# Kernel optimization log

Hardware: AMD Instinct MI355X
Metric: run time of the kernel (lower is better)

## Reference

```python
import jax, jax.numpy as jnp
import numpy as np


def setup_inputs() -> dict:
    key = jax.random.key(0)
    ks = jax.random.split(key, 16)
    B, S, H = 512, 128, 256
    f32 = jnp.float32
    inputs = jax.random.normal(ks[0], (B, S, 2), f32)
    # xavier-normal-ish init (gain/sqrt(fan_in+fan_out) approximated by small scale)
    def xn(k, shape):
        fan = shape[0] + shape[1]
        return jax.random.normal(k, shape, f32) * np.sqrt(2.0 / fan)
    return {
        "inputs": inputs,
        "W0": xn(ks[1], (H, 2)),   "b0": jnp.zeros((H,), f32),
        "W1": xn(ks[2], (H, H)),   "b1": jnp.zeros((H,), f32),
        "W2": xn(ks[3], (H, H)),   "b2": jnp.zeros((H,), f32),
        "W3": xn(ks[4], (H, H)),   "b3": jnp.zeros((H,), f32),
        "W4": xn(ks[5], (1, H)),   "b4": jnp.zeros((1,), f32),
        "log_growth_rate": jax.random.normal(ks[6], (), f32),
        "log_carrying_capacity": jax.random.normal(ks[7], (), f32),
        "log_initial_loss": jax.random.normal(ks[8], (), f32),
        "in_mean": jnp.array([0.5, 50.0], f32),
        "in_std": jnp.array([0.2, 30.0], f32),
        "tgt_mean": jnp.array([0.8], f32),
        "tgt_std": jnp.array([0.1], f32),
    }


def reference(inputs, W0, b0, W1, b1, W2, b2, W3, b3, W4, b4,
              log_growth_rate, log_carrying_capacity, log_initial_loss,
              in_mean, in_std, tgt_mean, tgt_std):
    B, S = inputs.shape[0], inputs.shape[1]
    # PDE parameters (Verhulst logistic growth)
    r = jnp.exp(-log_growth_rate)
    K = 0.2 + (1.0 - 0.2) * jax.nn.sigmoid(log_carrying_capacity)  # carrying capacity in [0.2, 1]
    C = 0.0 + (0.1 - 0.0) * jax.nn.sigmoid(log_initial_loss)       # initial loss in [0, 0.1]

    # split state feature s and time t, standardize per-column
    s = inputs[..., 0:1].reshape(-1, 1)  # [N,1]
    t = inputs[..., 1:2].reshape(-1, 1)  # [N,1]
    s_norm = (s - in_mean[0:1]) / (in_std[0:1] + 1e-8)
    t_norm = (t - in_mean[1:2]) / (in_std[1:2] + 1e-8)

    Ws = (W0, W1, W2, W3, W4)
    bs = (b0, b1, b2, b3, b4)

    def mlp(x):  # [N,2] -> [N,1], tanh MLP
        h = x
        for W, b in zip(Ws[:-1], bs[:-1]):
            h = jnp.tanh(h @ W.T + b)
        return h @ Ws[-1].T + bs[-1]

    def u_of(tn):  # U(s_norm, tn), inverse-standardized targets
        return mlp(jnp.concatenate([s_norm, tn], axis=-1)) * tgt_std + tgt_mean

    ones = jnp.ones_like(t_norm)

    def uf_of(tn):
        # U and U_t = dU/dt_norm (forward-mode; each point depends on its own scalar t)
        U, U_dot = jax.jvp(u_of, (tn,), (ones,))
        U_t = U_dot.sum(-1, keepdims=True)
        G = r * (U - C) * (1.0 - (U - C) / (K - C))  # Verhulst
        return U, U_t - G  # (U, F)

    # second derivative w.r.t. t_norm: F_t = U_tt - G_t
    (U, F), (_, F_t) = jax.jvp(uf_of, (t_norm,), (ones,))

    shp = (B, S, 1)
    return U.reshape(shp), F.reshape(shp), F_t.reshape(shp)
```

## Files before the change

kernel.cpp:

```cpp
#include <hip/hip_runtime.h>
#include <hip/hip_bf16.h>
#include <math.h>

typedef short s8v __attribute__((ext_vector_type(8)));
typedef float f4v __attribute__((ext_vector_type(4)));

#define HH 256
#define TP 32
#define NTHREADS 256
#define KSTR 520
#define TSTR 4160
#define NTILES 6
#define PLANE (NTILES * TSTR)

__device__ __forceinline__ unsigned short bf_rne(float x){
    union{float f;unsigned u;}v; v.f=x;
    unsigned r = v.u + 0x7FFFu + ((v.u >> 16) & 1u);
    return (unsigned short)(r >> 16);
}
__device__ __forceinline__ unsigned pack_rne2(float a, float b){
    union { __hip_bfloat162 h; unsigned u; } v;
    v.h = __float22bfloat162_rn(float2{a, b});
    return v.u;
}

__global__ __launch_bounds__(256)
void prep_weights(const float* __restrict__ W1, const float* __restrict__ W2,
                  const float* __restrict__ W3, const float* __restrict__ W0,
                  const float* __restrict__ b0, const float* __restrict__ W4,
                  unsigned short* __restrict__ wsB, float* __restrict__ wsF)
{
    int t = blockIdx.x * 256 + threadIdx.x;
    if (t < 24576) {
        int layer = t >> 13;
        int rem = t & 8191;
        int l  = rem & 63;
        int ks = (rem >> 6) & 7;
        int nt = rem >> 9;
        const float* W = (layer == 0) ? W1 : (layer == 1) ? W2 : W3;
        int n_out = nt * 16 + (l & 15);
        int quad  = l >> 4;
        const float* row = W + n_out * HH;
        s8v hi;
        #pragma unroll
        for (int j = 0; j < 8; ++j) {
            int n_in = quad * 64 + (j & 3) * 16 + ((j >> 2) << 3) + ks;
            hi[j] = (short)bf_rne(row[n_in]);
        }
        int dst = ((nt * 8 + ks) * 64 + l) * 8;
        *(s8v*)(wsB + layer * 65536 + dst) = hi;
    } else if (t < 24832) {
        int n = t - 24576;
        int pos = ((n & 7) * 4 + (n >> 6)) * 8 + ((n >> 4) & 3) + 4 * ((n >> 3) & 1);
        wsF[pos]       = W0[2 * n];
        wsF[256 + pos] = W0[2 * n + 1];
        wsF[512 + pos] = b0[n];
        wsF[768 + pos] = W4[n];
    }
}

__global__ __launch_bounds__(NTHREADS, 3)
void capnn_mfma(const float* __restrict__ inp,
                const float* __restrict__ b1, const float* __restrict__ b2,
                const float* __restrict__ b3, const float* __restrict__ b4,
                const float* __restrict__ W4raw,
                const float* __restrict__ lgr, const float* __restrict__ lcc,
                const float* __restrict__ lil,
                const float* __restrict__ imean, const float* __restrict__ istd,
                const float* __restrict__ tmean, const float* __restrict__ tstd,
                const unsigned short* __restrict__ wsW,
                const float* __restrict__ wsF,
                float* __restrict__ out, int N)
{
    __shared__ __align__(16) unsigned short Ahi[PLANE];
    __shared__ float sn_sh[TP], tn_sh[TP];
    __shared__ float head_part[TP * 3 * 4];

    const int tid  = threadIdx.x;
    const int lane = tid & 63;
    const int w    = tid >> 6;
    const int m16  = lane & 15;
    const int q    = lane >> 4;
    const int pbase = blockIdx.x * TP;

    const float* __restrict__ w00p = wsF;
    const float* __restrict__ w01p = wsF + 256;
    const float* __restrict__ b0p  = wsF + 512;

    float w4v[4];
    #pragma unroll
    for (int i = 0; i < 4; ++i) w4v[i] = W4raw[w * 64 + i * 16 + m16];

    if (tid < TP) {
        int pg = pbase + tid;
        float s = 0.f, t = 0.f;
        if (pg < N) { s = inp[2 * pg]; t = inp[2 * pg + 1]; }
        sn_sh[tid] = (s - imean[0]) / (istd[0] + 1e-8f);
        tn_sh[tid] = (t - imean[1]) / (istd[1] + 1e-8f);
    }
    __syncthreads();

    {
        const int l  = tid & 63;
        const int wv = tid >> 6;
        const int p16 = l & 15, quad = l >> 4;
        #pragma unroll
        for (int g2 = 0; g2 < 2; ++g2) {
            const int ks = wv + 4 * g2;
            const int pos = (ks * 4 + quad) * 8;
            float4 wA0 = *(const float4*)(w00p + pos);
            float4 wA1 = *(const float4*)(w00p + pos + 4);
            float4 wB0 = *(const float4*)(w01p + pos);
            float4 wB1 = *(const float4*)(w01p + pos + 4);
            float4 bb0 = *(const float4*)(b0p + pos);
            float4 bb1 = *(const float4*)(b0p + pos + 4);
            float w00v[8] = {wA0.x,wA0.y,wA0.z,wA0.w,wA1.x,wA1.y,wA1.z,wA1.w};
            float w01v[8] = {wB0.x,wB0.y,wB0.z,wB0.w,wB1.x,wB1.y,wB1.z,wB1.w};
            float b0v[8]  = {bb0.x,bb0.y,bb0.z,bb0.w,bb1.x,bb1.y,bb1.z,bb1.w};
            const int base = ks * KSTR + l * 8;
            #pragma unroll
            for (int h = 0; h < 2; ++h) {
                const float sn = sn_sh[h * 16 + p16], tn = tn_sh[h * 16 + p16];
                float av[8], d1v[8], d2v[8];
                #pragma unroll
                for (int j = 0; j < 8; ++j) {
                    float z = fmaf(w00v[j], sn, fmaf(w01v[j], tn, b0v[j]));
                    float e = __expf(2.f * z);
                    float a = 1.f - 2.f * __builtin_amdgcn_rcpf(e + 1.f);
                    float g = 1.f - a * a;
                    float d1 = g * w01v[j];
                    float d2 = -2.f * a * d1 * w01v[j];
                    av[j] = a; d1v[j] = d1; d2v[j] = d2;
                }
                #pragma unroll
                for (int s = 0; s < 3; ++s) {
                    const float* V = (s == 0) ? av : (s == 1) ? d1v : d2v;
                    int4 hi4;
                    hi4.x = (int)pack_rne2(V[0], V[1]);
                    hi4.y = (int)pack_rne2(V[2], V[3]);
                    hi4.z = (int)pack_rne2(V[4], V[5]);
                    hi4.w = (int)pack_rne2(V[6], V[7]);
                    *(int4*)&Ahi[(s * 2 + h) * TSTR + base] = hi4;
                }
            }
        }
    }
    __syncthreads();

    for (int L = 0; L < 3; ++L) {
        const unsigned short* __restrict__ Wlh = wsW + L * 65536;
        const float* __restrict__ bL = (L == 0) ? b1 : (L == 1) ? b2 : b3;

        f4v acc[NTILES][4];
        #pragma unroll
        for (int i = 0; i < 4; ++i) {
            float bias = bL[w * 64 + i * 16 + m16];
            acc[0][i] = (f4v){bias, bias, bias, bias};
            acc[1][i] = (f4v){bias, bias, bias, bias};
            #pragma unroll
            for (int t = 2; t < NTILES; ++t)
                acc[t][i] = (f4v){0.f, 0.f, 0.f, 0.f};
        }

        #pragma unroll
        for (int ks = 0; ks < 8; ++ks) {
            s8v ah[NTILES];
            const int aoff = ks * KSTR + lane * 8;
            #pragma unroll
            for (int t = 0; t < NTILES; ++t)
                ah[t] = *(const s8v*)&Ahi[t * TSTR + aoff];
            #pragma unroll
            for (int i = 0; i < 4; ++i) {
                const int off = (((w * 4 + i) * 8 + ks) * 64 + lane) * 8;
                s8v bh = *(const s8v*)(Wlh + off);
                #pragma unroll
                for (int t = 0; t < NTILES; ++t)
                    acc[t][i] = __builtin_amdgcn_mfma_f32_16x16x32_bf16(ah[t], bh, acc[t][i], 0, 0, 0);
            }
        }

        if (L < 2) {
            __syncthreads();
            const int ksw  = m16 & 7;
            const int hsel = m16 >> 3;
            const int wbase = ksw * KSTR + (16 * w + q * 4) * 8 + 4 * hsel;
            #pragma unroll
            for (int h = 0; h < 2; ++h) {
                #pragma unroll
                for (int r = 0; r < 4; ++r) {
                    float Av[3][4];
                    #pragma unroll
                    for (int i = 0; i < 4; ++i) {
                        float z  = acc[h][i][r];
                        float z1 = acc[2 + h][i][r];
                        float z2 = acc[4 + h][i][r];
                        float e = __expf(2.f * z);
                        float a = 1.f - 2.f * __builtin_amdgcn_rcpf(e + 1.f);
                        float g = 1.f - a * a;
                        float d1 = g * z1;
                        float d2 = fmaf(g, z2, -2.f * a * d1 * z1);
                        Av[0][i] = a; Av[1][i] = d1; Av[2][i] = d2;
                    }
                    #pragma unroll
                    for (int s = 0; s < 3; ++s) {
                        int2 hi2;
                        hi2.x = (int)pack_rne2(Av[s][0], Av[s][1]);
                        hi2.y = (int)pack_rne2(Av[s][2], Av[s][3]);
                        *(int2*)&Ahi[(s * 2 + h) * TSTR + wbase + r * 8] = hi2;
                    }
                }
            }
            __syncthreads();
        } else {
            float hp[3][2][4];
            #pragma unroll
            for (int s = 0; s < 3; ++s)
                #pragma unroll
                for (int h = 0; h < 2; ++h)
                    #pragma unroll
                    for (int r = 0; r < 4; ++r) hp[s][h][r] = 0.f;
            #pragma unroll
            for (int h = 0; h < 2; ++h) {
                #pragma unroll
                for (int r = 0; r < 4; ++r) {
                    #pragma unroll
                    for (int i = 0; i < 4; ++i) {
                        float z  = acc[h][i][r];
                        float z1 = acc[2 + h][i][r];
                        float z2 = acc[4 + h][i][r];
                        float e = __expf(2.f * z);
                        float a = 1.f - 2.f * __builtin_amdgcn_rcpf(e + 1.f);
                        float g = 1.f - a * a;
                        float d1 = g * z1;
                        float d2 = fmaf(g, z2, -2.f * a * d1 * z1);
                        hp[0][h][r] = fmaf(w4v[i], a,  hp[0][h][r]);
                        hp[1][h][r] = fmaf(w4v[i], d1, hp[1][h][r]);
                        hp[2][h][r] = fmaf(w4v[i], d2, hp[2][h][r]);
                    }
                }
            }
            #pragma unroll
            for (int m = 1; m < 16; m <<= 1) {
                #pragma unroll
                for (int s = 0; s < 3; ++s)
                    #pragma unroll
                    for (int h = 0; h < 2; ++h)
                        #pragma unroll
                        for (int r = 0; r < 4; ++r)
                            hp[s][h][r] += __shfl_xor(hp[s][h][r], m);
            }
            if (m16 == 0) {
                #pragma unroll
                for (int s = 0; s < 3; ++s)
                    #pragma unroll
                    for (int h = 0; h < 2; ++h)
                        #pragma unroll
                        for (int r = 0; r < 4; ++r)
                            head_part[(s * TP + h * 16 + q * 4 + r) * 4 + w] = hp[s][h][r];
            }
            __syncthreads();
        }
    }

    if (tid < TP) {
        float sv = 0.f, s1v = 0.f, s2v = 0.f;
        #pragma unroll
        for (int ww = 0; ww < 4; ++ww) {
            sv  += head_part[(0 * TP + tid) * 4 + ww];
            s1v += head_part[(1 * TP + tid) * 4 + ww];
            s2v += head_part[(2 * TP + tid) * 4 + ww];
        }
        int pg = pbase + tid;
        if (pg < N) {
            float r_  = expf(-lgr[0]);
            float Kc  = 0.2f + 0.8f / (1.f + expf(-lcc[0]));
            float Cc  = 0.1f / (1.f + expf(-lil[0]));
            float kci = 1.f / (Kc - Cc);
            float ts = tstd[0], tm = tmean[0];
            float U   = (sv + b4[0]) * ts + tm;
            float Ut  = s1v * ts;
            float Utt = s2v * ts;
            float Um  = U - Cc;
            float G   = r_ * Um * (1.f - Um * kci);
            float Gt  = r_ * Ut * (1.f - 2.f * Um * kci);
            out[pg]         = U;
            out[N + pg]     = Ut - G;
            out[2 * N + pg] = Utt - Gt;
        }
    }
}

extern "C" void kernel_launch(void* const* d_in, const int* in_sizes, int n_in,
                              void* d_out, int out_size, void* d_ws, size_t ws_size,
                              hipStream_t stream) {
    const float* inp   = (const float*)d_in[0];
    const float* W0    = (const float*)d_in[1];
    const float* b0    = (const float*)d_in[2];
    const float* W1    = (const float*)d_in[3];
    const float* b1    = (const float*)d_in[4];
    const float* W2    = (const float*)d_in[5];
    const float* b2    = (const float*)d_in[6];
    const float* W3    = (const float*)d_in[7];
    const float* b3    = (const float*)d_in[8];
    const float* W4    = (const float*)d_in[9];
    const float* b4    = (const float*)d_in[10];
    const float* lgr   = (const float*)d_in[11];
    const float* lcc   = (const float*)d_in[12];
    const float* lil   = (const float*)d_in[13];
    const float* imean = (const float*)d_in[14];
    const float* istd  = (const float*)d_in[15];
    const float* tmean = (const float*)d_in[16];
    const float* tstd  = (const float*)d_in[17];

    unsigned short* wsB = (unsigned short*)d_ws;
    float* wsF = (float*)((char*)d_ws + 393216);

    const int N = in_sizes[0] / 2;
    const int gridMain = (N + TP - 1) / TP;

    hipLaunchKernelGGL(prep_weights, dim3(97), dim3(256), 0, stream,
                       W1, W2, W3, W0, b0, W4, wsB, wsF);
    hipLaunchKernelGGL(capnn_mfma, dim3(gridMain), dim3(NTHREADS), 0, stream,
                       inp, b1, b2, b3, b4, W4,
                       lgr, lcc, lil, imean, istd, tmean, tstd,
                       wsB, wsF, (float*)d_out, N);
}
```

Baseline: 176.4 us.

## Ping-pong two wave sets staggered by one phase to overlap MFMA and tanh

The block now has 512 threads in two sets of four waves, each set working on its own 32-point tile with its own LDS plane. The sets run the layer schedule one phase apart, so one set's MFMA GEMM runs while the other does tanh/derivative elementwise work, and GEMM phases raise wave priority with s_setprio. This is meant to fill MFMA idle time during the transcendental-heavy epilogues, at the cost of double LDS use, lower declared occupancy (2 blocks) and a barrier every phase.

After: 184.8 us. 4.7% more time.

```diff
diff --git a/kernel.cpp b/kernel.cpp
--- a/kernel.cpp
+++ b/kernel.cpp
@@ -6,8 +6,9 @@
 typedef float f4v __attribute__((ext_vector_type(4)));
 
 #define HH 256
-#define TP 32
-#define NTHREADS 256
+#define TPS 32
+#define TP 64
+#define NTHREADS 512
 #define KSTR 520
 #define TSTR 4160
 #define NTILES 6
@@ -59,7 +60,7 @@
     }
 }
 
-__global__ __launch_bounds__(NTHREADS, 3)
+__global__ __launch_bounds__(NTHREADS, 2)
 void capnn_mfma(const float* __restrict__ inp,
                 const float* __restrict__ b1, const float* __restrict__ b2,
                 const float* __restrict__ b3, const float* __restrict__ b4,
@@ -72,27 +73,26 @@
                 const float* __restrict__ wsF,
                 float* __restrict__ out, int N)
 {
-    __shared__ __align__(16) unsigned short Ahi[PLANE];
+    __shared__ __align__(16) unsigned short Ahi[2 * PLANE];
     __shared__ float sn_sh[TP], tn_sh[TP];
-    __shared__ float head_part[TP * 3 * 4];
+    __shared__ float head_part[2][TPS * 3 * 4];
 
     const int tid  = threadIdx.x;
     const int lane = tid & 63;
     const int w    = tid >> 6;
+    const int set  = w >> 2;
+    const int wl   = w & 3;
     const int m16  = lane & 15;
     const int q    = lane >> 4;
-    const int pbase = blockIdx.x * TP;
+
+    unsigned short* const plane = Ahi + set * PLANE;
 
     const float* __restrict__ w00p = wsF;
     const float* __restrict__ w01p = wsF + 256;
     const float* __restrict__ b0p  = wsF + 512;
 
-    float w4v[4];
-    #pragma unroll
-    for (int i = 0; i < 4; ++i) w4v[i] = W4raw[w * 64 + i * 16 + m16];
-
     if (tid < TP) {
-        int pg = pbase + tid;
+        int pg = blockIdx.x * TP + tid;
         float s = 0.f, t = 0.f;
         if (pg < N) { s = inp[2 * pg]; t = inp[2 * pg + 1]; }
         sn_sh[tid] = (s - imean[0]) / (istd[0] + 1e-8f);
@@ -100,90 +100,93 @@
     }
     __syncthreads();
 
-    {
-        const int l  = tid & 63;
-        const int wv = tid >> 6;
-        const int p16 = l & 15, quad = l >> 4;
-        #pragma unroll
-        for (int g2 = 0; g2 < 2; ++g2) {
-            const int ks = wv + 4 * g2;
-            const int pos = (ks * 4 + quad) * 8;
-            float4 wA0 = *(const float4*)(w00p + pos);
-            float4 wA1 = *(const float4*)(w00p + pos + 4);
-            float4 wB0 = *(const float4*)(w01p + pos);
-            float4 wB1 = *(const float4*)(w01p + pos + 4);
-            float4 bb0 = *(const float4*)(b0p + pos);
-            float4 bb1 = *(const float4*)(b0p + pos + 4);
-            float w00v[8] = {wA0.x,wA0.y,wA0.z,wA0.w,wA1.x,wA1.y,wA1.z,wA1.w};
-            float w01v[8] = {wB0.x,wB0.y,wB0.z,wB0.w,wB1.x,wB1.y,wB1.z,wB1.w};
-            float b0v[8]  = {bb0.x,bb0.y,bb0.z,bb0.w,bb1.x,bb1.y,bb1.z,bb1.w};
-            const int base = ks * KSTR + l * 8;
-            #pragma unroll
-            for (int h = 0; h < 2; ++h) {
-                const float sn = sn_sh[h * 16 + p16], tn = tn_sh[h * 16 + p16];
-                float av[8], d1v[8], d2v[8];
-                #pragma unroll
-                for (int j = 0; j < 8; ++j) {
-                    float z = fmaf(w00v[j], sn, fmaf(w01v[j], tn, b0v[j]));
-                    float e = __expf(2.f * z);
-                    float a = 1.f - 2.f * __builtin_amdgcn_rcpf(e + 1.f);
-                    float g = 1.f - a * a;
-                    float d1 = g * w01v[j];
-                    float d2 = -2.f * a * d1 * w01v[j];
-                    av[j] = a; d1v[j] = d1; d2v[j] = d2;
+    f4v acc[NTILES][4];
+
+    #pragma unroll 1
+    for (int iv = 0; iv < 8; ++iv) {
+        const int ph = iv - set;
+
+        if (ph == 0) {
+            const int l = lane;
+            const int p16 = l & 15, quad = l >> 4;
+            #pragma unroll
+            for (int g2 = 0; g2 < 2; ++g2) {
+                const int ks = wl + 4 * g2;
+                const int pos = (ks * 4 + quad) * 8;
+                float4 wA0 = *(const float4*)(w00p + pos);
+                float4 wA1 = *(const float4*)(w00p + pos + 4);
+                float4 wB0 = *(const float4*)(w01p + pos);
+                float4 wB1 = *(const float4*)(w01p + pos + 4);
+                float4 bb0 = *(const float4*)(b0p + pos);
+                float4 bb1 = *(const float4*)(b0p + pos + 4);
+                float w00v[8] = {wA0.x,wA0.y,wA0.z,wA0.w,wA1.x,wA1.y,wA1.z,wA1.w};
+                float w01v[8] = {wB0.x,wB0.y,wB0.z,wB0.w,wB1.x,wB1.y,wB1.z,wB1.w};
+                float b0v[8]  = {bb0.x,bb0.y,bb0.z,bb0.w,bb1.x,bb1.y,bb1.z,bb1.w};
+                const int base = ks * KSTR + l * 8;
+                #pragma unroll
+                for (int h = 0; h < 2; ++h) {
+                    const float sn = sn_sh[set * TPS + h * 16 + p16];
+                    const float tn = tn_sh[set * TPS + h * 16 + p16];
+                    float av[8], d1v[8], d2v[8];
+                    #pragma unroll
+                    for (int j = 0; j < 8; ++j) {
+                        float z = fmaf(w00v[j], sn, fmaf(w01v[j], tn, b0v[j]));
+                        float e = __expf(2.f * z);
+                        float a = 1.f - 2.f * __builtin_amdgcn_rcpf(e + 1.f);
+                        float g = 1.f - a * a;
+                        float d1 = g * w01v[j];
+                        float d2 = -2.f * a * d1 * w01v[j];
+                        av[j] = a; d1v[j] = d1; d2v[j] = d2;
+                    }
+                    #pragma unroll
+                    for (int s = 0; s < 3; ++s) {
+                        const float* V = (s == 0) ? av : (s == 1) ? d1v : d2v;
+                        int4 hi4;
+                        hi4.x = (int)pack_rne2(V[0], V[1]);
+                        hi4.y = (int)pack_rne2(V[2], V[3]);
+                        hi4.z = (int)pack_rne2(V[4], V[5]);
+                        hi4.w = (int)pack_rne2(V[6], V[7]);
+                        *(int4*)&plane[(s * 2 + h) * TSTR + base] = hi4;
+                    }
                 }
-                #pragma unroll
-                for (int s = 0; s < 3; ++s) {
-                    const float* V = (s == 0) ? av : (s == 1) ? d1v : d2v;
-                    int4 hi4;
-                    hi4.x = (int)pack_rne2(V[0], V[1]);
-                    hi4.y = (int)pack_rne2(V[2], V[3]);
-                    hi4.z = (int)pack_rne2(V[4], V[5]);
-                    hi4.w = (int)pack_rne2(V[6], V[7]);
-                    *(int4*)&Ahi[(s * 2 + h) * TSTR + base] = hi4;
+            }
+        } else if (ph == 1 || ph == 3 || ph == 5) {
+            const int L = (ph - 1) >> 1;
+            const unsigned short* __restrict__ Wlh = wsW + L * 65536;
+            const float* __restrict__ bL = (L == 0) ? b1 : (L == 1) ? b2 : b3;
+
+            #pragma unroll
+            for (int i = 0; i < 4; ++i) {
+                float bias = bL[wl * 64 + i * 16 + m16];
+                acc[0][i] = (f4v){bias, bias, bias, bias};
+                acc[1][i] = (f4v){bias, bias, bias, bias};
+                #pragma unroll
+                for (int t = 2; t < NTILES; ++t)
+                    acc[t][i] = (f4v){0.f, 0.f, 0.f, 0.f};
+            }
+
+            __builtin_amdgcn_s_setprio(1);
+            #pragma unroll
+            for (int ks = 0; ks < 8; ++ks) {
+                s8v ah[NTILES];
+                const int aoff = ks * KSTR + lane * 8;
+                #pragma unroll
+                for (int t = 0; t < NTILES; ++t)
+                    ah[t] = *(const s8v*)&plane[t * TSTR + aoff];
+                #pragma unroll
+                for (int i = 0; i < 4; ++i) {
+                    const int off = (((wl * 4 + i) * 8 + ks) * 64 + lane) * 8;
+                    s8v bh = *(const s8v*)(Wlh + off);
+                    #pragma unroll
+                    for (int t = 0; t < NTILES; ++t)
+                        acc[t][i] = __builtin_amdgcn_mfma_f32_16x16x32_bf16(ah[t], bh, acc[t][i], 0, 0, 0);
                 }
             }
-        }
-    }
-    __syncthreads();
-
-    for (int L = 0; L < 3; ++L) {
-        const unsigned short* __restrict__ Wlh = wsW + L * 65536;
-        const float* __restrict__ bL = (L == 0) ? b1 : (L == 1) ? b2 : b3;
-
-        f4v acc[NTILES][4];
-        #pragma unroll
-        for (int i = 0; i < 4; ++i) {
-            float bias = bL[w * 64 + i * 16 + m16];
-            acc[0][i] = (f4v){bias, bias, bias, bias};
-            acc[1][i] = (f4v){bias, bias, bias, bias};
-            #pragma unroll
-            for (int t = 2; t < NTILES; ++t)
-                acc[t][i] = (f4v){0.f, 0.f, 0.f, 0.f};
-        }
-
-        #pragma unroll
-        for (int ks = 0; ks < 8; ++ks) {
-            s8v ah[NTILES];
-            const int aoff = ks * KSTR + lane * 8;
-            #pragma unroll
-            for (int t = 0; t < NTILES; ++t)
-                ah[t] = *(const s8v*)&Ahi[t * TSTR + aoff];
-            #pragma unroll
-            for (int i = 0; i < 4; ++i) {
-                const int off = (((w * 4 + i) * 8 + ks) * 64 + lane) * 8;
-                s8v bh = *(const s8v*)(Wlh + off);
-                #pragma unroll
-                for (int t = 0; t < NTILES; ++t)
-                    acc[t][i] = __builtin_amdgcn_mfma_f32_16x16x32_bf16(ah[t], bh, acc[t][i], 0, 0, 0);
-            }
-        }
-
-        if (L < 2) {
-            __syncthreads();
+            __builtin_amdgcn_s_setprio(0);
+        } else if (ph == 2 || ph == 4) {
             const int ksw  = m16 & 7;
             const int hsel = m16 >> 3;
-            const int wbase = ksw * KSTR + (16 * w + q * 4) * 8 + 4 * hsel;
+            const int wbase = ksw * KSTR + (16 * wl + q * 4) * 8 + 4 * hsel;
             #pragma unroll
             for (int h = 0; h < 2; ++h) {
                 #pragma unroll
@@ -206,12 +209,15 @@
                         int2 hi2;
                         hi2.x = (int)pack_rne2(Av[s][0], Av[s][1]);
                         hi2.y = (int)pack_rne2(Av[s][2], Av[s][3]);
-                        *(int2*)&Ahi[(s * 2 + h) * TSTR + wbase + r * 8] = hi2;
+                        *(int2*)&plane[(s * 2 + h) * TSTR + wbase + r * 8] = hi2;
                     }
                 }
             }
-            __syncthreads();
-        } else {
+        } else if (ph == 6) {
+            float w4v[4];
+            #pragma unroll
+            for (int i = 0; i < 4; ++i) w4v[i] = W4raw[wl * 64 + i * 16 + m16];
+
             float hp[3][2][4];
             #pragma unroll
             for (int s = 0; s < 3; ++s)
@@ -256,21 +262,23 @@
                     for (int h = 0; h < 2; ++h)
                         #pragma unroll
                         for (int r = 0; r < 4; ++r)
-                            head_part[(s * TP + h * 16 + q * 4 + r) * 4 + w] = hp[s][h][r];
-            }
-            __syncthreads();
+                            head_part[set][(s * TPS + h * 16 + q * 4 + r) * 4 + wl] = hp[s][h][r];
+            }
         }
+        __syncthreads();
     }
 
     if (tid < TP) {
+        const int sset = tid >> 5;
+        const int pl   = tid & 31;
         float sv = 0.f, s1v = 0.f, s2v = 0.f;
         #pragma unroll
         for (int ww = 0; ww < 4; ++ww) {
-            sv  += head_part[(0 * TP + tid) * 4 + ww];
-            s1v += head_part[(1 * TP + tid) * 4 + ww];
-            s2v += head_part[(2 * TP + tid) * 4 + ww];
+            sv  += head_part[sset][(0 * TPS + pl) * 4 + ww];
+            s1v += head_part[sset][(1 * TPS + pl) * 4 + ww];
+            s2v += head_part[sset][(2 * TPS + pl) * 4 + ww];
         }
-        int pg = pbase + tid;
+        int pg = blockIdx.x * TP + tid;
         if (pg < N) {
             float r_  = expf(-lgr[0]);
             float Kc  = 0.2f + 0.8f / (1.f + expf(-lcc[0]));
```

## Halve points per block to one 16-row tile and double occupancy

Applied to the files above, without the earlier changes.

Cuts each block from 32 to 16 points, so there are three MFMA row tiles (value, first and second derivative) instead of six. This halves the accumulator registers and LDS per block, which allows launch bounds of 6 blocks per CU. It also raises wave priority around the MFMA loop with s_setprio. The trade-off is that every B-fragment weight load now feeds half as many MFMAs, doubling weight traffic per point, and the grid has twice as many blocks.

Measured after the change: 296.0 us. +67.8%, slower.

```diff
diff --git a/kernel.cpp b/kernel.cpp
--- a/kernel.cpp
+++ b/kernel.cpp
@@ -6,11 +6,11 @@
 typedef float f4v __attribute__((ext_vector_type(4)));
 
 #define HH 256
-#define TP 32
+#define TP 16
 #define NTHREADS 256
 #define KSTR 520
 #define TSTR 4160
-#define NTILES 6
+#define NTILES 3
 #define PLANE (NTILES * TSTR)
 
 __device__ __forceinline__ unsigned short bf_rne(float x){
@@ -59,7 +59,7 @@
     }
 }
 
-__global__ __launch_bounds__(NTHREADS, 3)
+__global__ __launch_bounds__(NTHREADS, 6)
 void capnn_mfma(const float* __restrict__ inp,
                 const float* __restrict__ b1, const float* __restrict__ b2,
                 const float* __restrict__ b3, const float* __restrict__ b4,
@@ -101,12 +101,12 @@
     __syncthreads();
 
     {
-        const int l  = tid & 63;
-        const int wv = tid >> 6;
+        const int l  = lane;
         const int p16 = l & 15, quad = l >> 4;
+        const float sn = sn_sh[p16], tn = tn_sh[p16];
         #pragma unroll
         for (int g2 = 0; g2 < 2; ++g2) {
-            const int ks = wv + 4 * g2;
+            const int ks = w + 4 * g2;
             const int pos = (ks * 4 + quad) * 8;
             float4 wA0 = *(const float4*)(w00p + pos);
             float4 wA1 = *(const float4*)(w00p + pos + 4);
@@ -118,30 +118,26 @@
             float w01v[8] = {wB0.x,wB0.y,wB0.z,wB0.w,wB1.x,wB1.y,wB1.z,wB1.w};
             float b0v[8]  = {bb0.x,bb0.y,bb0.z,bb0.w,bb1.x,bb1.y,bb1.z,bb1.w};
             const int base = ks * KSTR + l * 8;
-            #pragma unroll
-            for (int h = 0; h < 2; ++h) {
-                const float sn = sn_sh[h * 16 + p16], tn = tn_sh[h * 16 + p16];
-                float av[8], d1v[8], d2v[8];
-                #pragma unroll
-                for (int j = 0; j < 8; ++j) {
-                    float z = fmaf(w00v[j], sn, fmaf(w01v[j], tn, b0v[j]));
-                    float e = __expf(2.f * z);
-                    float a = 1.f - 2.f * __builtin_amdgcn_rcpf(e + 1.f);
-                    float g = 1.f - a * a;
-                    float d1 = g * w01v[j];
-                    float d2 = -2.f * a * d1 * w01v[j];
-                    av[j] = a; d1v[j] = d1; d2v[j] = d2;
-                }
-                #pragma unroll
-                for (int s = 0; s < 3; ++s) {
-                    const float* V = (s == 0) ? av : (s == 1) ? d1v : d2v;
-                    int4 hi4;
-                    hi4.x = (int)pack_rne2(V[0], V[1]);
-                    hi4.y = (int)pack_rne2(V[2], V[3]);
-                    hi4.z = (int)pack_rne2(V[4], V[5]);
-                    hi4.w = (int)pack_rne2(V[6], V[7]);
-                    *(int4*)&Ahi[(s * 2 + h) * TSTR + base] = hi4;
-                }
+            float av[8], d1v[8], d2v[8];
+            #pragma unroll
+            for (int j = 0; j < 8; ++j) {
+                float z = fmaf(w00v[j], sn, fmaf(w01v[j], tn, b0v[j]));
+                float e = __expf(2.f * z);
+                float a = 1.f - 2.f * __builtin_amdgcn_rcpf(e + 1.f);
+                float g = 1.f - a * a;
+                float d1 = g * w01v[j];
+                float d2 = -2.f * a * d1 * w01v[j];
+                av[j] = a; d1v[j] = d1; d2v[j] = d2;
+            }
+            #pragma unroll
+            for (int s = 0; s < 3; ++s) {
+                const float* V = (s == 0) ? av : (s == 1) ? d1v : d2v;
+                int4 hi4;
+                hi4.x = (int)pack_rne2(V[0], V[1]);
+                hi4.y = (int)pack_rne2(V[2], V[3]);
+                hi4.z = (int)pack_rne2(V[4], V[5]);
+                hi4.w = (int)pack_rne2(V[6], V[7]);
+                *(int4*)&Ahi[s * TSTR + base] = hi4;
             }
         }
     }
@@ -156,12 +152,11 @@
         for (int i = 0; i < 4; ++i) {
             float bias = bL[w * 64 + i * 16 + m16];
             acc[0][i] = (f4v){bias, bias, bias, bias};
-            acc[1][i] = (f4v){bias, bias, bias, bias};
-            #pragma unroll
-            for (int t = 2; t < NTILES; ++t)
-                acc[t][i] = (f4v){0.f, 0.f, 0.f, 0.f};
-        }
-
+            acc[1][i] = (f4v){0.f, 0.f, 0.f, 0.f};
+            acc[2][i] = (f4v){0.f, 0.f, 0.f, 0.f};
+        }
+
+        __builtin_amdgcn_s_setprio(1);
         #pragma unroll
         for (int ks = 0; ks < 8; ++ks) {
             s8v ah[NTILES];
@@ -178,6 +173,7 @@
                     acc[t][i] = __builtin_amdgcn_mfma_f32_16x16x32_bf16(ah[t], bh, acc[t][i], 0, 0, 0);
             }
         }
+        __builtin_amdgcn_s_setprio(0);
 
         if (L < 2) {
             __syncthreads();
@@ -185,58 +181,50 @@
             const int hsel = m16 >> 3;
             const int wbase = ksw * KSTR + (16 * w + q * 4) * 8 + 4 * hsel;
             #pragma unroll
-            for (int h = 0; h < 2; ++h) {
-                #pragma unroll
-                for (int r = 0; r < 4; ++r) {
-                    float Av[3][4];
-                    #pragma unroll
-                    for (int i = 0; i < 4; ++i) {
-                        float z  = acc[h][i][r];
-                        float z1 = acc[2 + h][i][r];
-                        float z2 = acc[4 + h][i][r];
-                        float e = __expf(2.f * z);
-                        float a = 1.f - 2.f * __builtin_amdgcn_rcpf(e + 1.f);
-                        float g = 1.f - a * a;
-                        float d1 = g * z1;
-                        float d2 = fmaf(g, z2, -2.f * a * d1 * z1);
-                        Av[0][i] = a; Av[1][i] = d1; Av[2][i] = d2;
-                    }
-                    #pragma unroll
-                    for (int s = 0; s < 3; ++s) {
-                        int2 hi2;
-                        hi2.x = (int)pack_rne2(Av[s][0], Av[s][1]);
-                        hi2.y = (int)pack_rne2(Av[s][2], Av[s][3]);
-                        *(int2*)&Ahi[(s * 2 + h) * TSTR + wbase + r * 8] = hi2;
-                    }
+            for (int r = 0; r < 4; ++r) {
+                float Av[3][4];
+                #pragma unroll
+                for (int i = 0; i < 4; ++i) {
+                    float z  = acc[0][i][r];
+                    float z1 = acc[1][i][r];
+                    float z2 = acc[2][i][r];
+                    float e = __expf(2.f * z);
+                    float a = 1.f - 2.f * __builtin_amdgcn_rcpf(e + 1.f);
+                    float g = 1.f - a * a;
+                    float d1 = g * z1;
+                    float d2 = fmaf(g, z2, -2.f * a * d1 * z1);
+                    Av[0][i] = a; Av[1][i] = d1; Av[2][i] = d2;
+                }
+                #pragma unroll
+                for (int s = 0; s < 3; ++s) {
+                    int2 hi2;
+                    hi2.x = (int)pack_rne2(Av[s][0], Av[s][1]);
+                    hi2.y = (int)pack_rne2(Av[s][2], Av[s][3]);
+                    *(int2*)&Ahi[s * TSTR + wbase + r * 8] = hi2;
                 }
             }
             __syncthreads();
         } else {
-            float hp[3][2][4];
+            float hp[3][4];
             #pragma unroll
             for (int s = 0; s < 3; ++s)
                 #pragma unroll
-                for (int h = 0; h < 2; ++h)
-                    #pragma unroll
-                    for (int r = 0; r < 4; ++r) hp[s][h][r] = 0.f;
-            #pragma unroll
-            for (int h = 0; h < 2; ++h) {
-                #pragma unroll
-                for (int r = 0; r < 4; ++r) {
-                    #pragma unroll
-                    for (int i = 0; i < 4; ++i) {
-                        float z  = acc[h][i][r];
-                        float z1 = acc[2 + h][i][r];
-                        float z2 = acc[4 + h][i][r];
-                        float e = __expf(2.f * z);
-                        float a = 1.f - 2.f * __builtin_amdgcn_rcpf(e + 1.f);
-                        float g = 1.f - a * a;
-                        float d1 = g * z1;
-                        float d2 = fmaf(g, z2, -2.f * a * d1 * z1);
-                        hp[0][h][r] = fmaf(w4v[i], a,  hp[0][h][r]);
-                        hp[1][h][r] = fmaf(w4v[i], d1, hp[1][h][r]);
-                        hp[2][h][r] = fmaf(w4v[i], d2, hp[2][h][r]);
-                    }
+                for (int r = 0; r < 4; ++r) hp[s][r] = 0.f;
+            #pragma unroll
+            for (int r = 0; r < 4; ++r) {
+                #pragma unroll
+                for (int i = 0; i < 4; ++i) {
+                    float z  = acc[0][i][r];
+                    float z1 = acc[1][i][r];
+                    float z2 = acc[2][i][r];
+                    float e = __expf(2.f * z);
+                    float a = 1.f - 2.f * __builtin_amdgcn_rcpf(e + 1.f);
+                    float g = 1.f - a * a;
+                    float d1 = g * z1;
+                    float d2 = fmaf(g, z2, -2.f * a * d1 * z1);
+                    hp[0][r] = fmaf(w4v[i], a,  hp[0][r]);
+                    hp[1][r] = fmaf(w4v[i], d1, hp[1][r]);
+                    hp[2][r] = fmaf(w4v[i], d2, hp[2][r]);
                 }
             }
             #pragma unroll
@@ -244,19 +232,15 @@
                 #pragma unroll
                 for (int s = 0; s < 3; ++s)
                     #pragma unroll
-                    for (int h = 0; h < 2; ++h)
-                        #pragma unroll
-                        for (int r = 0; r < 4; ++r)
-                            hp[s][h][r] += __shfl_xor(hp[s][h][r], m);
+                    for (int r = 0; r < 4; ++r)
+                        hp[s][r] += __shfl_xor(hp[s][r], m);
             }
             if (m16 == 0) {
                 #pragma unroll
                 for (int s = 0; s < 3; ++s)
                     #pragma unroll
-                    for (int h = 0; h < 2; ++h)
-                        #pragma unroll
-                        for (int r = 0; r < 4; ++r)
-                            head_part[(s * TP + h * 16 + q * 4 + r) * 4 + w] = hp[s][h][r];
+                    for (int r = 0; r < 4; ++r)
+                        head_part[(s * TP + q * 4 + r) * 4 + w] = hp[s][r];
             }
             __syncthreads();
         }
```
